# Optimization experiments

Hardware: AMD Instinct MI355X
Metric: run time of the kernel (lower is better)

Reference implementation:

```python
import jax, jax.numpy as jnp
import numpy as np

T, B, I, H, P, O = 512, 256, 64, 128, 256, 50
NUM_LAYERS = 2
BN_EPS = 1e-5


def _gru_scan(xs, h0, Wih, Whh, bih, bhh):
    # xs: [T, B, in]; precompute input projections for all steps at once
    xp = jnp.einsum('tbi,gi->tbg', xs, Wih) + bih  # [T, B, 3H]

    def step(h, x_t):
        gh = h @ Whh.T + bhh                      # [B, 3H]
        xr, xz, xn = jnp.split(x_t, 3, axis=-1)
        hr, hz, hn = jnp.split(gh, 3, axis=-1)
        r = jax.nn.sigmoid(xr + hr)
        z = jax.nn.sigmoid(xz + hz)
        n = jnp.tanh(xn + r * hn)
        h_new = (1.0 - z) * n + z * h
        return h_new, h_new

    _, ys = jax.lax.scan(step, h0, xp)
    return ys  # [T, B, H]


def setup_inputs() -> dict:
    key = jax.random.key(0)
    ks = jax.random.split(key, 24)
    s = 0.05
    inp = {
        'x': jax.random.normal(ks[0], (T, B, I), dtype=jnp.float32),
        'h0': jnp.zeros((NUM_LAYERS, B, H), dtype=jnp.float32),
        # GRU layer 0 (input I -> H)
        'Wih0': jax.random.normal(ks[1], (3 * H, I)) * s,
        'Whh0': jax.random.normal(ks[2], (3 * H, H)) * s,
        'bih0': jax.random.normal(ks[3], (3 * H,)) * s,
        'bhh0': jax.random.normal(ks[4], (3 * H,)) * s,
        # GRU layer 1 (input H -> H)
        'Wih1': jax.random.normal(ks[5], (3 * H, H)) * s,
        'Whh1': jax.random.normal(ks[6], (3 * H, H)) * s,
        'bih1': jax.random.normal(ks[7], (3 * H,)) * s,
        'bhh1': jax.random.normal(ks[8], (3 * H,)) * s,
        # proj Linear H -> P
        'Wp': jax.random.normal(ks[9], (P, H)) * s,
        'bp': jax.random.normal(ks[10], (P,)) * s,
        # BatchNorm1d(P) affine params (training-mode batch stats)
        'gamma': jnp.ones((P,), dtype=jnp.float32),
        'beta': jnp.zeros((P,), dtype=jnp.float32),
        # GRUCell P -> P
        'Wcih': jax.random.normal(ks[11], (3 * P, P)) * s,
        'Wchh': jax.random.normal(ks[12], (3 * P, P)) * s,
        'bcih': jax.random.normal(ks[13], (3 * P,)) * s,
        'bchh': jax.random.normal(ks[14], (3 * P,)) * s,
        # input skip Linear I -> P
        'Ws': jax.random.normal(ks[15], (P, I)) * s,
        'bs': jax.random.normal(ks[16], (P,)) * s,
        # final Linear P -> O
        'Wf': jax.random.normal(ks[17], (O, P)) * s,
        'bf': jax.random.normal(ks[18], (O,)) * s,
    }
    return inp


def reference(x, h0, Wih0, Whh0, bih0, bhh0, Wih1, Whh1, bih1, bhh1,
              Wp, bp, gamma, beta, Wcih, Wchh, bcih, bchh, Ws, bs, Wf, bf):
    # two-layer unidirectional GRU
    y0 = _gru_scan(x, h0[0], Wih0, Whh0, bih0, bhh0)   # [T, B, H]
    rnn_out = _gru_scan(y0, h0[1], Wih1, Whh1, bih1, bhh1)  # [T, B, H]

    # linear projection to proj_dim
    proj_seq = jnp.einsum('tbh,ph->tbp', rnn_out, Wp) + bp  # [T, B, P]

    # BatchNorm1d in training mode over flattened (batch*time), per-feature
    mean = jnp.mean(proj_seq, axis=(0, 1))
    var = jnp.mean((proj_seq - mean) ** 2, axis=(0, 1))  # biased variance
    bn_seq = gamma * (proj_seq - mean) * jax.lax.rsqrt(var + BN_EPS) + beta

    # sequential GRUCell refinement over time, GELU on each step's state
    cell_h0 = jnp.zeros((x.shape[1], Wchh.shape[1]), dtype=bn_seq.dtype)
    cell_states = _gru_scan(bn_seq, cell_h0, Wcih, Wchh, bcih, bchh)  # [T, B, P]
    refined_seq = jax.nn.gelu(cell_states, approximate=False)

    # residual skip from raw input
    skip_seq = jnp.einsum('tbi,pi->tbp', x, Ws) + bs

    aggregated = jnp.mean(refined_seq + skip_seq, axis=0)  # [B, P]
    out = aggregated @ Wf.T + bf                            # [B, O]
    return out
```

## Files before the change

### kernel.cpp

```cpp
#include <hip/hip_runtime.h>

#define T_DIM 512
#define B_DIM 256
#define I_DIM 64
#define H_DIM 128
#define P_DIM 256
#define O_DIM 50

typedef _Float16 half8 __attribute__((ext_vector_type(8)));
typedef _Float16 half4 __attribute__((ext_vector_type(4)));
typedef float f32x4 __attribute__((ext_vector_type(4)));

#define GLOAD_LDS16(G, L)                                                      \
  __builtin_amdgcn_global_load_lds(                                            \
      (const __attribute__((address_space(1))) void*)(G),                      \
      (__attribute__((address_space(3))) void*)(L), 16, 0, 0)

__device__ __forceinline__ float sigm(float x) {
  return __builtin_amdgcn_rcpf(1.f + __expf(-x));
}
__device__ __forceinline__ float tanh_f(float x) {
  x = fminf(20.f, fmaxf(-20.f, x));
  float e = __expf(2.f * x);
  return (e - 1.f) * __builtin_amdgcn_rcpf(e + 1.f);
}

__global__ void cvt_k(const float* __restrict__ s, _Float16* __restrict__ d, long n) {
  long i = (long)blockIdx.x * blockDim.x + threadIdx.x;
  long st = (long)gridDim.x * blockDim.x;
  for (; i < n; i += st) d[i] = (_Float16)s[i];
}

__global__ void xmean_k(const float* __restrict__ x, float* __restrict__ xm) {
  int b = blockIdx.x, i = threadIdx.x;
  float s = 0.f;
  for (int t = 0; t < T_DIM; ++t) s += x[((long)t * B_DIM + b) * I_DIM + i];
  xm[b * I_DIM + i] = s * (1.0f / T_DIM);
}

__global__ void skip_k(const float* __restrict__ xm, const float* __restrict__ Wsk,
                       const float* __restrict__ bsk, float* __restrict__ skipm) {
  int b = blockIdx.x, p = threadIdx.x;
  float s = bsk[p];
  for (int i = 0; i < I_DIM; ++i) s += xm[b * I_DIM + i] * Wsk[p * I_DIM + i];
  skipm[b * P_DIM + p] = s;
}

__global__ void zero2_k(float* a, float* b2) {
  int p = threadIdx.x;
  a[p] = 0.f;
  b2[p] = 0.f;
}

__global__ void zeroN_k(float* a, int n) {
  int i = blockIdx.x * blockDim.x + threadIdx.x;
  if (i < n) a[i] = 0.f;
}

__global__ void stats_k(const _Float16* __restrict__ proj, float* __restrict__ gsum,
                        float* __restrict__ gss) {
  int p = threadIdx.x;
  long r0 = (long)blockIdx.x * 256;
  float s = 0.f, ss = 0.f;
  for (int r = 0; r < 256; ++r) {
    float v = (float)proj[(r0 + r) * P_DIM + p];
    s += v;
    ss += v * v;
  }
  atomicAdd(&gsum[p], s);
  atomicAdd(&gss[p], ss);
}

__global__ void bnprep_k(const float* gsum, const float* gss, const float* gamma,
                         const float* beta, float* bns, float* bnt) {
  int p = threadIdx.x;
  const float inv = 1.0f / ((float)T_DIM * (float)B_DIM);
  float m = gsum[p] * inv;
  float v = gss[p] * inv - m * m;
  float rs = rsqrtf(v + 1e-5f);
  float s = gamma[p] * rs;
  bns[p] = s;
  bnt[p] = beta[p] - m * s;
}

__global__ void fold_k(const float* __restrict__ Wcih, const float* __restrict__ bcih,
                       const float* __restrict__ bns, const float* __restrict__ bnt,
                       _Float16* __restrict__ WF, float* __restrict__ bF) {
  __shared__ float red[256];
  int n = blockIdx.x, k = threadIdx.x;
  float wv = Wcih[n * 256 + k];
  WF[n * 256 + k] = (_Float16)(wv * bns[k]);
  red[k] = wv * bnt[k];
  __syncthreads();
  for (int s = 128; s > 0; s >>= 1) {
    if (k < s) red[k] += red[k + s];
    __syncthreads();
  }
  if (k == 0) bF[n] = bcih[n] + red[0];
}

__global__ __launch_bounds__(256) void gemm_k(
    const _Float16* __restrict__ A, const _Float16* __restrict__ W,
    const float* __restrict__ bias, const float* __restrict__ bias2, int n2lim,
    _Float16* __restrict__ C, int M, int N, int K, int transN) {
  __shared__ __align__(16) _Float16 As[128 * 64];
  __shared__ __align__(16) _Float16 Bs[128 * 64];
  const int tid = threadIdx.x;
  const int l = tid & 63;
  const int w = tid >> 6;
  const int wr = w >> 1, wc = w & 1;
  const int lrow = l & 15, lk = l >> 4;
  const long bm = blockIdx.x, bn = blockIdx.y;

  f32x4 z = {0.f, 0.f, 0.f, 0.f};
  f32x4 acc[4][4];
#pragma unroll
  for (int m = 0; m < 4; ++m)
#pragma unroll
    for (int n = 0; n < 4; ++n) acc[m][n] = z;

  for (int k0 = 0; k0 < K; k0 += 64) {
    if (k0) __syncthreads();
#pragma unroll
    for (int it = 0; it < 4; ++it) {
      const int lin = it * 256 + tid;
      const int row = lin >> 3, slot = lin & 7;
      const int scol = (slot ^ (row & 7)) << 3;
      GLOAD_LDS16(A + (bm * 128 + row) * (long)K + k0 + scol, (_Float16*)As + (size_t)lin * 8);
      GLOAD_LDS16(W + (bn * 128 + row) * (long)K + k0 + scol, (_Float16*)Bs + (size_t)lin * 8);
    }
    __syncthreads();
#pragma unroll
    for (int kk = 0; kk < 2; ++kk) {
      half8 af[4], wfr[4];
#pragma unroll
      for (int m = 0; m < 4; ++m) {
        const int row = wr * 64 + m * 16 + lrow;
        af[m] = *(const half8*)((const char*)As +
                                ((row * 128 + (kk * 32 + lk * 8) * 2) ^ ((row & 7) << 4)));
      }
#pragma unroll
      for (int n = 0; n < 4; ++n) {
        const int row = wc * 64 + n * 16 + lrow;
        wfr[n] = *(const half8*)((const char*)Bs +
                                 ((row * 128 + (kk * 32 + lk * 8) * 2) ^ ((row & 7) << 4)));
      }
#pragma unroll
      for (int m = 0; m < 4; ++m)
#pragma unroll
        for (int n = 0; n < 4; ++n)
          acc[m][n] = __builtin_amdgcn_mfma_f32_16x16x32_f16(af[m], wfr[n], acc[m][n], 0, 0, 0);
    }
  }
  if (transN) {
    const long tIdx = bm >> 1;
    const long TCH = M >> 8;
#pragma unroll
    for (int n = 0; n < 4; ++n) {
      const int gn = (int)bn * 128 + wc * 64 + n * 16 + lrow;
      float bv = 0.f;
      if (bias) bv += bias[gn];
      if (bias2 && gn < n2lim) bv += bias2[gn];
#pragma unroll
      for (int m = 0; m < 4; ++m) {
        half4 v;
#pragma unroll
        for (int r = 0; r < 4; ++r) v[r] = (_Float16)(acc[m][n][r] + bv);
        const int blk = (int)(bm & 1) * 8 + wr * 4 + m;
        *(half4*)(C + ((blk * TCH + tIdx) * N + gn) * 16 + lk * 4) = v;
      }
    }
  } else {
#pragma unroll
    for (int n = 0; n < 4; ++n) {
      const int gn = (int)bn * 128 + wc * 64 + n * 16 + lrow;
      float bv = 0.f;
      if (bias) bv += bias[gn];
      if (bias2 && gn < n2lim) bv += bias2[gn];
#pragma unroll
      for (int m = 0; m < 4; ++m)
#pragma unroll
        for (int r = 0; r < 4; ++r) {
          const long gm = bm * 128 + wr * 64 + m * 16 + lk * 4 + r;
          C[gm * (long)N + gn] = (_Float16)(acc[m][n][r] + bv);
        }
    }
  }
}

__global__ __launch_bounds__(512, 1) void scan01_pipe(
    const _Float16* __restrict__ xp0T,
    const _Float16* __restrict__ Whh0h,
    const _Float16* __restrict__ Wih1h,
    const _Float16* __restrict__ Whh1h,
    const float* __restrict__ bhh0, const float* __restrict__ bih1,
    const float* __restrict__ bhh1,
    const float* __restrict__ h0init,
    _Float16* __restrict__ y0buf,
    _Float16* __restrict__ h1buf,
    int* flags) {
  __shared__ __align__(16) _Float16 hL[2][16 * 128];
  const int tid = threadIdx.x;
  const int l = tid & 63, w = tid >> 6;
  const int lrow = l & 15, lk = l >> 4;
  const int bblk = blockIdx.x & 15;
  const int rbase = bblk * 16;
  const int p = w * 16 + lrow;

  if (blockIdx.x < 16) {
    half8 wf0[3][4];
#pragma unroll
    for (int g = 0; g < 3; ++g)
#pragma unroll
      for (int kk = 0; kk < 4; ++kk)
        wf0[g][kk] = *(const half8*)(Whh0h + (size_t)(g * 128 + p) * 128 + kk * 32 + lk * 8);
    const float bN0 = bhh0[2 * H_DIM + p];
    float h0r[4];
#pragma unroll
    for (int r = 0; r < 4; ++r) h0r[r] = h0init[(rbase + lk * 4 + r) * H_DIM + p];
    for (int i = tid; i < 16 * 128; i += 512) {
      int row = i >> 7, pp = i & 127;
      int byte = (row * 256 + pp * 2) ^ ((row & 7) << 4);
      *(_Float16*)((char*)hL[1] + byte) = (_Float16)h0init[(rbase + row) * H_DIM + pp];
    }
    __syncthreads();

    half4 xA[3], xB[3];
    auto loadx = [&](half4(&X)[3], int tt) {
#pragma unroll
      for (int g = 0; g < 3; ++g)
        X[g] = *(const half4*)(xp0T + (((long)bblk * T_DIM + tt) * 384 + g * 128 + p) * 16 +
                               lk * 4);
    };
    auto pstep = [&](int t, half4(&XC)[3], half4(&XN)[3]) {
      loadx(XN, (t + 1 < T_DIM) ? t + 1 : T_DIM - 1);
      char* cur = (char*)hL[(t & 1) ^ 1];
      char* nxt = (char*)hL[t & 1];
      half8 af[4];
#pragma unroll
      for (int kk = 0; kk < 4; ++kk) {
        int byte = (lrow * 256 + (kk * 32 + lk * 8) * 2) ^ ((lrow & 7) << 4);
        af[kk] = *(const half8*)(cur + byte);
      }
      f32x4 aR, aZ, aN;
#pragma unroll
      for (int r = 0; r < 4; ++r) {
        aR[r] = (float)XC[0][r];
        aZ[r] = (float)XC[1][r];
        aN[r] = 0.f;
      }
#pragma unroll
      for (int kk = 0; kk < 4; ++kk) {
        aR = __builtin_amdgcn_mfma_f32_16x16x32_f16(af[kk], wf0[0][kk], aR, 0, 0, 0);
        aZ = __builtin_amdgcn_mfma_f32_16x16x32_f16(af[kk], wf0[1][kk], aZ, 0, 0, 0);
        aN = __builtin_amdgcn_mfma_f32_16x16x32_f16(af[kk], wf0[2][kk], aN, 0, 0, 0);
      }
#pragma unroll
      for (int r = 0; r < 4; ++r) {
        float rg = sigm(aR[r]);
        float zg = sigm(aZ[r]);
        float ng = tanh_f((float)XC[2][r] + rg * (aN[r] + bN0));
        float hv = ng + zg * (h0r[r] - ng);
        h0r[r] = hv;
        int row = lk * 4 + r;
        int byte = (row * 256 + p * 2) ^ ((row & 7) << 4);
        *(_Float16*)(nxt + byte) = (_Float16)hv;
        y0buf[((size_t)(bblk * T_DIM + t) * 16 + row) * 128 + p] = (_Float16)hv;
      }
      if ((t & 3) == 3) {
        __threadfence();
        __syncthreads();
        if (tid == 0)
          __hip_atomic_store(&flags[bblk], t + 1, __ATOMIC_RELEASE, __HIP_MEMORY_SCOPE_AGENT);
      } else {
        __syncthreads();
      }
    };
    loadx(xA, 0);
    for (int t = 0; t < T_DIM; t += 2) {
      pstep(t, xA, xB);
      pstep(t + 1, xB, xA);
    }
  } else {
    half8 wf1x[3][4], wf1h[3][4];
#pragma unroll
    for (int g = 0; g < 3; ++g)
#pragma unroll
      for (int kk = 0; kk < 4; ++kk) {
        const size_t ro = (size_t)(g * 128 + p) * 128 + kk * 32 + lk * 8;
        wf1x[g][kk] = *(const half8*)(Wih1h + ro);
        wf1h[g][kk] = *(const half8*)(Whh1h + ro);
      }
    const float bR1 = bih1[p] + bhh1[p];
    const float bZ1 = bih1[H_DIM + p] + bhh1[H_DIM + p];
    const float bX1 = bih1[2 * H_DIM + p];
    const float bN1 = bhh1[2 * H_DIM + p];
    float h1r[4];
#pragma unroll
    for (int r = 0; r < 4; ++r)
      h1r[r] = h0init[B_DIM * H_DIM + (rbase + lk * 4 + r) * H_DIM + p];
    for (int i = tid; i < 16 * 128; i += 512) {
      int row = i >> 7, pp = i & 127;
      int byte = (row * 256 + pp * 2) ^ ((row & 7) << 4);
      *(_Float16*)((char*)hL[1] + byte) =
          (_Float16)h0init[B_DIM * H_DIM + (rbase + row) * H_DIM + pp];
    }
    __syncthreads();

    const _Float16* yb = y0buf + (size_t)bblk * T_DIM * 16 * 128;
    int avail = 0;
    auto wait_for = [&](int target) {
      if (avail < target) {
        do {
          __builtin_amdgcn_s_sleep(2);
          avail = __hip_atomic_load(&flags[bblk], __ATOMIC_ACQUIRE, __HIP_MEMORY_SCOPE_AGENT);
        } while (avail < target);
      }
    };
    auto loady = [&](half8(&Y)[4], int tt) {
#pragma unroll
      for (int kk = 0; kk < 4; ++kk)
        Y[kk] = *(const half8*)(yb + ((size_t)tt * 16 + lrow) * 128 + kk * 32 + lk * 8);
    };
    auto cstep = [&](int t, half8(&YC)[4], half8(&YN)[4]) {
      wait_for((t + 2 < T_DIM) ? (t + 2) : T_DIM);
      loady(YN, (t + 1 < T_DIM) ? t + 1 : T_DIM - 1);
      char* cur = (char*)hL[(t & 1) ^ 1];
      char* nxt = (char*)hL[t & 1];
      f32x4 aRx = {bR1, bR1, bR1, bR1};
      f32x4 aZx = {bZ1, bZ1, bZ1, bZ1};
      f32x4 aX = {bX1, bX1, bX1, bX1};
      f32x4 aRh = {0.f, 0.f, 0.f, 0.f};
      f32x4 aZh = {0.f, 0.f, 0.f, 0.f};
      f32x4 aH = {0.f, 0.f, 0.f, 0.f};
      half8 ah[4];
#pragma unroll
      for (int kk = 0; kk < 4; ++kk) {
        int byte = (lrow * 256 + (kk * 32 + lk * 8) * 2) ^ ((lrow & 7) << 4);
        ah[kk] = *(const half8*)(cur + byte);
      }
#pragma unroll
      for (int kk = 0; kk < 4; ++kk) {
        aRx = __builtin_amdgcn_mfma_f32_16x16x32_f16(YC[kk], wf1x[0][kk], aRx, 0, 0, 0);
        aZx = __builtin_amdgcn_mfma_f32_16x16x32_f16(YC[kk], wf1x[1][kk], aZx, 0, 0, 0);
        aX = __builtin_amdgcn_mfma_f32_16x16x32_f16(YC[kk], wf1x[2][kk], aX, 0, 0, 0);
        aRh = __builtin_amdgcn_mfma_f32_16x16x32_f16(ah[kk], wf1h[0][kk], aRh, 0, 0, 0);
        aZh = __builtin_amdgcn_mfma_f32_16x16x32_f16(ah[kk], wf1h[1][kk], aZh, 0, 0, 0);
        aH = __builtin_amdgcn_mfma_f32_16x16x32_f16(ah[kk], wf1h[2][kk], aH, 0, 0, 0);
      }
#pragma unroll
      for (int r = 0; r < 4; ++r) {
        float rg = sigm(aRx[r] + aRh[r]);
        float zg = sigm(aZx[r] + aZh[r]);
        float ng = tanh_f(aX[r] + rg * (aH[r] + bN1));
        float hv = ng + zg * (h1r[r] - ng);
        h1r[r] = hv;
        int row = lk * 4 + r;
        int byte = (row * 256 + p * 2) ^ ((row & 7) << 4);
        *(_Float16*)(nxt + byte) = (_Float16)hv;
        h1buf[((long)t * B_DIM + rbase + row) * 128 + p] = (_Float16)hv;
      }
      __syncthreads();
    };
    half8 yA[4], yB[4];
    wait_for(2);
    loady(yA, 0);
    for (int t = 0; t < T_DIM; t += 2) {
      cstep(t, yA, yB);
      cstep(t + 1, yB, yA);
    }
  }
}

__global__ __launch_bounds__(512, 1) void scan_cell(
    const _Float16* __restrict__ xpT,
    _Float16* __restrict__ hT,
    float* __restrict__ hst, const _Float16* __restrict__ Whh,
    const float* __restrict__ bhh, int TC, int first) {
  __shared__ __align__(16) _Float16 hL[2][16 * 256];
  __shared__ __align__(16) _Float16 WL[768 * 64];
  const int tid = threadIdx.x;
  const int l = tid & 63, w = tid >> 6;
  const int lrow = l & 15, lk = l >> 4;
  const int rbase = blockIdx.x * 16;

  half8 wf[6][6];
#pragma unroll
  for (int g = 0; g < 3; ++g)
#pragma unroll
    for (int c = 0; c < 2; ++c) {
      const int nt = g * 16 + 2 * w + c;
#pragma unroll
      for (int kk = 0; kk < 6; ++kk)
        wf[g * 2 + c][kk] =
            *(const half8*)(Whh + (size_t)(nt * 16 + lrow) * P_DIM + kk * 32 + lk * 8);
    }
  for (int q = tid; q < 768 * 8; q += 512) {
    int row = q >> 3, slot = q & 7;
    int scol = (slot ^ (row & 7)) << 3;
    *(half8*)((char*)WL + (size_t)q * 16) = *(const half8*)(Whh + (size_t)row * P_DIM + 192 + scol);
  }
  float bN[2];
#pragma unroll
  for (int c = 0; c < 2; ++c) bN[c] = bhh[2 * P_DIM + 32 * w + 16 * c + lrow];

  float h[2][4];
#pragma unroll
  for (int c = 0; c < 2; ++c)
#pragma unroll
    for (int r = 0; r < 4; ++r)
      h[c][r] = first ? 0.f : hst[(rbase + lk * 4 + r) * P_DIM + 32 * w + 16 * c + lrow];
  for (int i = tid; i < 16 * 256; i += 512) {
    int row = i >> 8, pp = i & 255;
    float hv = first ? 0.f : hst[(rbase + row) * P_DIM + pp];
    int byte = (row * 512 + pp * 2) ^ ((row & 7) << 4);
    *(_Float16*)((char*)hL[0] + byte) = (_Float16)hv;
  }
  __syncthreads();

  half4 xA[3][2], xB[3][2];
  auto loadx = [&](half4(&X)[3][2], int tt) {
#pragma unroll
    for (int g = 0; g < 3; ++g)
#pragma unroll
      for (int c = 0; c < 2; ++c)
        X[g][c] = *(const half4*)(xpT +
                                  (((long)blockIdx.x * TC + tt) * 768 + g * 256 + 32 * w + 16 * c +
                                   lrow) * 16 + lk * 4);
  };
  auto step = [&](int tt, half4(&XC)[3][2], half4(&XN)[3][2], int tn) {
    loadx(XN, tn);
    char* hCur = (char*)hL[tt & 1];
    char* hNxt = (char*)hL[(tt & 1) ^ 1];
    half8 af[4];
    f32x4 acc[3][2];
#pragma unroll
    for (int c = 0; c < 2; ++c)
#pragma unroll
      for (int r = 0; r < 4; ++r) {
        acc[0][c][r] = (float)XC[0][c][r];
        acc[1][c][r] = (float)XC[1][c][r];
        acc[2][c][r] = 0.f;
      }
#pragma unroll
    for (int kk = 0; kk < 4; ++kk) {
      int byte = (lrow * 512 + (kk * 32 + lk * 8) * 2) ^ ((lrow & 7) << 4);
      af[kk] = *(const half8*)(hCur + byte);
    }
#pragma unroll
    for (int g = 0; g < 3; ++g)
#pragma unroll
      for (int c = 0; c < 2; ++c)
#pragma unroll
        for (int kk = 0; kk < 4; ++kk)
          acc[g][c] =
              __builtin_amdgcn_mfma_f32_16x16x32_f16(af[kk], wf[g * 2 + c][kk], acc[g][c], 0, 0, 0);
#pragma unroll
    for (int kk = 0; kk < 4; ++kk) {
      int byte = (lrow * 512 + ((kk + 4) * 32 + lk * 8) * 2) ^ ((lrow & 7) << 4);
      af[kk] = *(const half8*)(hCur + byte);
    }
#pragma unroll
    for (int g = 0; g < 3; ++g)
#pragma unroll
      for (int c = 0; c < 2; ++c) {
        const int nt = g * 16 + 2 * w + c;
        const int wrow = nt * 16 + lrow;
        f32x4 a = acc[g][c];
        a = __builtin_amdgcn_mfma_f32_16x16x32_f16(af[0], wf[g * 2 + c][4], a, 0, 0, 0);
        a = __builtin_amdgcn_mfma_f32_16x16x32_f16(af[1], wf[g * 2 + c][5], a, 0, 0, 0);
        half8 w6 = *(const half8*)((char*)WL + ((wrow * 128 + lk * 16) ^ ((wrow & 7) << 4)));
        half8 w7 = *(const half8*)((char*)WL + ((wrow * 128 + 64 + lk * 16) ^ ((wrow & 7) << 4)));
        a = __builtin_amdgcn_mfma_f32_16x16x32_f16(af[2], w6, a, 0, 0, 0);
        a = __builtin_amdgcn_mfma_f32_16x16x32_f16(af[3], w7, a, 0, 0, 0);
        acc[g][c] = a;
      }
#pragma unroll
    for (int c = 0; c < 2; ++c) {
      half4 hv4;
#pragma unroll
      for (int r = 0; r < 4; ++r) {
        float rg = sigm(acc[0][c][r]);
        float zg = sigm(acc[1][c][r]);
        float ng = tanh_f((float)XC[2][c][r] + rg * (acc[2][c][r] + bN[c]));
        float hv = ng + zg * (h[c][r] - ng);
        h[c][r] = hv;
        hv4[r] = (_Float16)hv;
        const int row = lk * 4 + r, pp = 32 * w + 16 * c + lrow;
        int byte = (row * 512 + pp * 2) ^ ((row & 7) << 4);
        *(_Float16*)(hNxt + byte) = hv4[r];
      }
      *(half4*)(hT + ((long)tt * 256 + 32 * w + 16 * c + lrow) * 256 + rbase + lk * 4) = hv4;
    }
    __syncthreads();
  };
  loadx(xA, 0);
  for (int t = 0; t < TC; t += 2) {
    step(t, xA, xB, t + 1);
    step(t + 1, xB, xA, (t + 2 < TC) ? t + 2 : TC - 1);
  }
#pragma unroll
  for (int c = 0; c < 2; ++c)
#pragma unroll
    for (int r = 0; r < 4; ++r)
      hst[(rbase + lk * 4 + r) * P_DIM + 32 * w + 16 * c + lrow] = h[c][r];
}

__global__ void gelu_mean_k(const _Float16* __restrict__ hT, float* __restrict__ aggT) {
  int p = blockIdx.x, b = threadIdx.x;
  int t0 = blockIdx.y * 64;
  float s = 0.f;
  for (int t = t0; t < t0 + 64; ++t) {
    float v = (float)hT[((long)t * P_DIM + p) * B_DIM + b];
    s += 0.5f * v * (1.f + erff(v * 0.70710678118f));
  }
  atomicAdd(&aggT[p * B_DIM + b], s);
}

__global__ void final_k(const float* __restrict__ aggT, const float* __restrict__ skipm,
                        const float* __restrict__ Wf, const float* __restrict__ bfb,
                        float* __restrict__ out) {
  int b = blockIdx.x, o = threadIdx.x;
  if (o >= O_DIM) return;
  float s = bfb[o];
  for (int p = 0; p < P_DIM; ++p)
    s += (aggT[p * B_DIM + b] * (1.0f / T_DIM) + skipm[b * P_DIM + p]) * Wf[o * P_DIM + p];
  out[b * O_DIM + o] = s;
}

extern "C" void kernel_launch(void* const* d_in, const int* in_sizes, int n_in, void* d_out,
                              int out_size, void* d_ws, size_t ws_size, hipStream_t stream) {
  const float* x = (const float*)d_in[0];
  const float* h0 = (const float*)d_in[1];
  const float* Wih0 = (const float*)d_in[2];
  const float* Whh0f = (const float*)d_in[3];
  const float* bih0 = (const float*)d_in[4];
  const float* bhh0 = (const float*)d_in[5];
  const float* Wih1 = (const float*)d_in[6];
  const float* Whh1f = (const float*)d_in[7];
  const float* bih1 = (const float*)d_in[8];
  const float* bhh1 = (const float*)d_in[9];
  const float* Wp = (const float*)d_in[10];
  const float* bp = (const float*)d_in[11];
  const float* gamma = (const float*)d_in[12];
  const float* beta = (const float*)d_in[13];
  const float* Wcih = (const float*)d_in[14];
  const float* Wchhf = (const float*)d_in[15];
  const float* bcih = (const float*)d_in[16];
  const float* bchh = (const float*)d_in[17];
  const float* Wsk = (const float*)d_in[18];
  const float* bsk = (const float*)d_in[19];
  const float* Wf = (const float*)d_in[20];
  const float* bfb = (const float*)d_in[21];
  float* out = (float*)d_out;

  char* wsp = (char*)d_ws;
  size_t off = 0;
  auto alloc = [&](size_t b) -> void* {
    void* p = wsp + off;
    off = (off + b + 255) & ~(size_t)255;
    return p;
  };
  _Float16* xh = (_Float16*)alloc((size_t)T_DIM * B_DIM * I_DIM * 2);
  _Float16* wih0 = (_Float16*)alloc(384 * 64 * 2);
  _Float16* whh0 = (_Float16*)alloc(384 * 128 * 2);
  _Float16* wih1 = (_Float16*)alloc(384 * 128 * 2);
  _Float16* whh1 = (_Float16*)alloc(384 * 128 * 2);
  _Float16* wp = (_Float16*)alloc(256 * 128 * 2);
  _Float16* wcihF = (_Float16*)alloc(768 * 256 * 2);
  _Float16* wchh = (_Float16*)alloc(768 * 256 * 2);
  _Float16* proj = (_Float16*)alloc((size_t)T_DIM * B_DIM * P_DIM * 2);
  _Float16* hT = (_Float16*)alloc((size_t)T_DIM * B_DIM * P_DIM * 2);
  float* hstc = (float*)alloc(B_DIM * P_DIM * 4);
  float* aggT = (float*)alloc(B_DIM * P_DIM * 4);
  float* xm = (float*)alloc(B_DIM * I_DIM * 4);
  float* skipm = (float*)alloc(B_DIM * P_DIM * 4);
  float* gsum = (float*)alloc(256 * 4);
  float* gss = (float*)alloc(256 * 4);
  float* bns = (float*)alloc(256 * 4);
  float* bnt = (float*)alloc(256 * 4);
  float* bcihF = (float*)alloc(768 * 4);
  int* flags = (int*)alloc(64 * 4);

  _Float16* y0buf = proj;
  _Float16* h1buf = hT;

  const size_t xp0_bytes = (size_t)T_DIM * 384 * B_DIM * 2;
  int TC2 = 512;
  while (TC2 > 32 && off + ((size_t)TC2 * B_DIM * 768 * 2 > xp0_bytes
                                ? (size_t)TC2 * B_DIM * 768 * 2
                                : xp0_bytes) >
                         ws_size)
    TC2 >>= 1;
  size_t xpb_bytes = (size_t)TC2 * B_DIM * 768 * 2;
  if (xpb_bytes < xp0_bytes) xpb_bytes = xp0_bytes;
  _Float16* xpb = (_Float16*)alloc(xpb_bytes);
  const int nc2 = T_DIM / TC2;
  const int M2 = TC2 * B_DIM;

  auto cvt = [&](const float* s, _Float16* d, long n) {
    long g = (n + 255) / 256;
    if (g > 2048) g = 2048;
    cvt_k<<<dim3((unsigned)g), dim3(256), 0, stream>>>(s, d, n);
  };
  cvt(x, xh, (long)T_DIM * B_DIM * I_DIM);
  cvt(Wih0, wih0, 384 * 64);
  cvt(Whh0f, whh0, 384 * 128);
  cvt(Wih1, wih1, 384 * 128);
  cvt(Whh1f, whh1, 384 * 128);
  cvt(Wp, wp, 256 * 128);
  cvt(Wchhf, wchh, 768 * 256);

  xmean_k<<<B_DIM, I_DIM, 0, stream>>>(x, xm);
  skip_k<<<B_DIM, P_DIM, 0, stream>>>(xm, Wsk, bsk, skipm);
  zero2_k<<<1, 256, 0, stream>>>(gsum, gss);
  zeroN_k<<<256, 256, 0, stream>>>(aggT, B_DIM * P_DIM);
  zeroN_k<<<1, 64, 0, stream>>>((float*)flags, 64);

  gemm_k<<<dim3(T_DIM * B_DIM / 128, 3), 256, 0, stream>>>(xh, wih0, bih0, bhh0, 2 * H_DIM, xpb,
                                                           T_DIM * B_DIM, 3 * H_DIM, I_DIM, 1);
  scan01_pipe<<<32, 512, 0, stream>>>(xpb, whh0, wih1, whh1, bhh0, bih1, bhh1, h0, y0buf, h1buf,
                                      flags);
  gemm_k<<<dim3(T_DIM * B_DIM / 128, 2), 256, 0, stream>>>(h1buf, wp, bp, (const float*)nullptr,
                                                           0, proj, T_DIM * B_DIM, P_DIM, H_DIM,
                                                           0);
  stats_k<<<512, 256, 0, stream>>>(proj, gsum, gss);
  bnprep_k<<<1, 256, 0, stream>>>(gsum, gss, gamma, beta, bns, bnt);
  fold_k<<<768, 256, 0, stream>>>(Wcih, bcih, bns, bnt, wcihF, bcihF);
  for (int c = 0; c < nc2; ++c) {
    const _Float16* pc = proj + (size_t)c * TC2 * B_DIM * P_DIM;
    gemm_k<<<dim3(M2 / 128, 6), 256, 0, stream>>>(pc, wcihF, bcihF, bchh, 2 * P_DIM, xpb, M2,
                                                  3 * P_DIM, P_DIM, 1);
    scan_cell<<<16, 512, 0, stream>>>(xpb, hT + (size_t)c * TC2 * B_DIM * P_DIM, hstc, wchh, bchh,
                                      TC2, c == 0);
  }
  gelu_mean_k<<<dim3(P_DIM, 8), B_DIM, 0, stream>>>(hT, aggT);
  final_k<<<B_DIM, 64, 0, stream>>>(aggT, skipm, Wf, bfb, out);
}
```

Measured before the change: 2.384 ms.

## Fuse projection GEMM and BN stats into pipelined scan kernel as consumer blocks

Adds 16 extra blocks to the layer-0/1 scan kernel. They wait on per-batch-block progress flags from layer 1, compute the Wp projection with MFMA, write proj, and accumulate the BatchNorm sum and sum of squares. This removes the separate projection GEMM and stats kernel launches and hides their work under the sequential scan. Layer-1 blocks now publish flags every 16 steps, which adds fence overhead, and y0buf is moved into the second half of hT to avoid aliasing proj.

```diff
diff --git a/kernel.cpp b/kernel.cpp
--- a/kernel.cpp
+++ b/kernel.cpp
@@ -55,20 +55,6 @@
 __global__ void zeroN_k(float* a, int n) {
   int i = blockIdx.x * blockDim.x + threadIdx.x;
   if (i < n) a[i] = 0.f;
-}
-
-__global__ void stats_k(const _Float16* __restrict__ proj, float* __restrict__ gsum,
-                        float* __restrict__ gss) {
-  int p = threadIdx.x;
-  long r0 = (long)blockIdx.x * 256;
-  float s = 0.f, ss = 0.f;
-  for (int r = 0; r < 256; ++r) {
-    float v = (float)proj[(r0 + r) * P_DIM + p];
-    s += v;
-    ss += v * v;
-  }
-  atomicAdd(&gsum[p], s);
-  atomicAdd(&gss[p], ss);
 }
 
 __global__ void bnprep_k(const float* gsum, const float* gss, const float* gamma,
@@ -193,12 +179,14 @@
     const _Float16* __restrict__ Whh0h,
     const _Float16* __restrict__ Wih1h,
     const _Float16* __restrict__ Whh1h,
+    const _Float16* __restrict__ Wph,
     const float* __restrict__ bhh0, const float* __restrict__ bih1,
-    const float* __restrict__ bhh1,
+    const float* __restrict__ bhh1, const float* __restrict__ bp,
     const float* __restrict__ h0init,
     _Float16* __restrict__ y0buf,
     _Float16* __restrict__ h1buf,
-    int* flags) {
+    _Float16* __restrict__ proj,
+    float* __restrict__ gsum, float* __restrict__ gss, int* flags) {
   __shared__ __align__(16) _Float16 hL[2][16 * 128];
   const int tid = threadIdx.x;
   const int l = tid & 63, w = tid >> 6;
@@ -281,7 +269,7 @@
       pstep(t, xA, xB);
       pstep(t + 1, xB, xA);
     }
-  } else {
+  } else if (blockIdx.x < 32) {
     half8 wf1x[3][4], wf1h[3][4];
 #pragma unroll
     for (int g = 0; g < 3; ++g)
@@ -360,7 +348,15 @@
         *(_Float16*)(nxt + byte) = (_Float16)hv;
         h1buf[((long)t * B_DIM + rbase + row) * 128 + p] = (_Float16)hv;
       }
-      __syncthreads();
+      if ((t & 15) == 15) {
+        __threadfence();
+        __syncthreads();
+        if (tid == 0)
+          __hip_atomic_store(&flags[16 + bblk], t + 1, __ATOMIC_RELEASE,
+                             __HIP_MEMORY_SCOPE_AGENT);
+      } else {
+        __syncthreads();
+      }
     };
     half8 yA[4], yB[4];
     wait_for(2);
@@ -368,6 +364,72 @@
     for (int t = 0; t < T_DIM; t += 2) {
       cstep(t, yA, yB);
       cstep(t + 1, yB, yA);
+    }
+  } else {
+    half8 wpf[2][4];
+#pragma unroll
+    for (int c = 0; c < 2; ++c)
+#pragma unroll
+      for (int kk = 0; kk < 4; ++kk)
+        wpf[c][kk] =
+            *(const half8*)(Wph + (size_t)(32 * w + 16 * c + lrow) * 128 + kk * 32 + lk * 8);
+    const float pb0 = bp[32 * w + lrow], pb1 = bp[32 * w + 16 + lrow];
+    float sm0 = 0.f, sm1 = 0.f, sq0 = 0.f, sq1 = 0.f;
+    int avail = 0;
+    auto wait_for = [&](int target) {
+      if (avail < target) {
+        do {
+          __builtin_amdgcn_s_sleep(8);
+          avail =
+              __hip_atomic_load(&flags[16 + bblk], __ATOMIC_ACQUIRE, __HIP_MEMORY_SCOPE_AGENT);
+        } while (avail < target);
+      }
+    };
+    for (int t0 = 0; t0 < T_DIM; t0 += 16) {
+      wait_for(t0 + 16);
+      for (int t = t0; t < t0 + 16; ++t) {
+        half8 ap[4];
+#pragma unroll
+        for (int kk = 0; kk < 4; ++kk)
+          ap[kk] = *(const half8*)(h1buf + ((long)t * B_DIM + rbase + lrow) * 128 + kk * 32 +
+                                   lk * 8);
+#pragma unroll
+        for (int c = 0; c < 2; ++c) {
+          const int prow = 32 * w + 16 * c + lrow;
+          float bv = c ? pb1 : pb0;
+          f32x4 pa = {bv, bv, bv, bv};
+#pragma unroll
+          for (int kk = 0; kk < 4; ++kk)
+            pa = __builtin_amdgcn_mfma_f32_16x16x32_f16(ap[kk], wpf[c][kk], pa, 0, 0, 0);
+#pragma unroll
+          for (int r = 0; r < 4; ++r) {
+            _Float16 pv = (_Float16)pa[r];
+            proj[((long)t * B_DIM + rbase + lk * 4 + r) * P_DIM + prow] = pv;
+            float pf = (float)pv;
+            if (c) {
+              sm1 += pf;
+              sq1 += pf * pf;
+            } else {
+              sm0 += pf;
+              sq0 += pf * pf;
+            }
+          }
+        }
+      }
+    }
+    sm0 += __shfl_xor(sm0, 16);
+    sm0 += __shfl_xor(sm0, 32);
+    sq0 += __shfl_xor(sq0, 16);
+    sq0 += __shfl_xor(sq0, 32);
+    sm1 += __shfl_xor(sm1, 16);
+    sm1 += __shfl_xor(sm1, 32);
+    sq1 += __shfl_xor(sq1, 16);
+    sq1 += __shfl_xor(sq1, 32);
+    if (lk == 0) {
+      atomicAdd(&gsum[32 * w + lrow], sm0);
+      atomicAdd(&gss[32 * w + lrow], sq0);
+      atomicAdd(&gsum[32 * w + 16 + lrow], sm1);
+      atomicAdd(&gss[32 * w + 16 + lrow], sq1);
     }
   }
 }
@@ -582,8 +644,8 @@
   float* bcihF = (float*)alloc(768 * 4);
   int* flags = (int*)alloc(64 * 4);
 
-  _Float16* y0buf = proj;
   _Float16* h1buf = hT;
+  _Float16* y0buf = hT + (size_t)T_DIM * B_DIM * 128;
 
   const size_t xp0_bytes = (size_t)T_DIM * 384 * B_DIM * 2;
   int TC2 = 512;
@@ -619,12 +681,9 @@
 
   gemm_k<<<dim3(T_DIM * B_DIM / 128, 3), 256, 0, stream>>>(xh, wih0, bih0, bhh0, 2 * H_DIM, xpb,
                                                            T_DIM * B_DIM, 3 * H_DIM, I_DIM, 1);
-  scan01_pipe<<<32, 512, 0, stream>>>(xpb, whh0, wih1, whh1, bhh0, bih1, bhh1, h0, y0buf, h1buf,
-                                      flags);
-  gemm_k<<<dim3(T_DIM * B_DIM / 128, 2), 256, 0, stream>>>(h1buf, wp, bp, (const float*)nullptr,
-                                                           0, proj, T_DIM * B_DIM, P_DIM, H_DIM,
-                                                           0);
-  stats_k<<<512, 256, 0, stream>>>(proj, gsum, gss);
+  scan01_pipe<<<48, 512, 0, stream>>>(xpb, whh0, wih1, whh1, wp, bhh0, bih1, bhh1, bp, h0, y0buf,
+                                      h1buf, proj, gsum, gss, flags);
+
   bnprep_k<<<1, 256, 0, stream>>>(gsum, gss, gamma, beta, bns, bnt);
   fold_k<<<768, 256, 0, stream>>>(Wcih, bcih, bns, bnt, wcihF, bcihF);
   for (int c = 0; c < nc2; ++c) {
```

Result: slower. 2.640 ms (+10.7%).
